# Optimization experiments

Measured on AMD Instinct MI355X. Metric: run time of the kernel, lower is better.

The kernel has to match this reference:

```python
import jax, jax.numpy as jnp
import numpy as np

GRID = (160, 160, 160)
RADIUS_FACTOR = 3.0
PATCH = 20      # fixed patch edge; covers ceil(c+r)-floor(c-r)+1 for r <= 9 voxels
CHUNK = 500
N_POINTS = 25000


def _quat_to_rot(q):
    # normalized quaternion -> rotation matrix (matches torch reference)
    q = q / jnp.clip(jnp.linalg.norm(q, axis=-1, keepdims=True), 1e-6)
    w, x, y, z = q[..., 0], q[..., 1], q[..., 2], q[..., 3]
    ww, xx, yy, zz = w * w, x * x, y * y, z * z
    wx, wy, wz = w * x, w * y, w * z
    xy, xz, yz = x * y, x * z, y * z
    r0 = jnp.stack([ww + xx - yy - zz, 2 * (xy - wz), 2 * (xz + wy)], -1)
    r1 = jnp.stack([2 * (xy + wz), ww - xx + yy - zz, 2 * (yz - wx)], -1)
    r2 = jnp.stack([2 * (xz - wy), 2 * (yz + wx), ww - xx - yy + zz], -1)
    return jnp.stack([r0, r1, r2], -2)


def setup_inputs():
    key = jax.random.key(0)
    k1, k2, k3, k4 = jax.random.split(key, 4)
    centers = jax.random.uniform(k1, (N_POINTS, 3), dtype=jnp.float32)
    # scales in [1.5, 3.0] voxels -> patch radius = 3*max(scale) <= 9 < PATCH/2
    log_scales = jnp.log(jax.random.uniform(k2, (N_POINTS, 3), minval=1.5, maxval=3.0, dtype=jnp.float32))
    quats = jax.random.normal(k3, (N_POINTS, 4), dtype=jnp.float32)
    rho = 0.1 * jax.random.normal(k4, (N_POINTS, 2), dtype=jnp.float32)  # (real, imag)
    return {"centers": centers, "log_scales": log_scales, "quats": quats, "rho": rho}


def _splat(centers, log_scales, quats, rho):
    D, H, W = GRID
    span = jnp.array([D - 1, H - 1, W - 1], jnp.float32)
    scales = jnp.exp(log_scales)                                  # [N,3]
    R = _quat_to_rot(quats)                                       # [N,3,3]
    inv = 1.0 / jnp.clip(scales, 1e-4) ** 2                       # diag of S^-2
    prec = jnp.einsum('nij,nj,nkj->nik', R, inv, R)               # R diag R^T, [N,3,3]
    cv = centers * span                                           # voxel-space centers
    rad = jnp.max(scales, axis=-1) * RADIUS_FACTOR                # per-point patch radius
    base = jnp.floor(cv - rad[:, None]).astype(jnp.int32)         # zmin/ymin/xmin (pre-clip)
    hi = jnp.ceil(cv + rad[:, None]).astype(jnp.int32)            # zmax/ymax/xmax (pre-clip)
    amp_mag = jnp.sqrt(rho[:, 0] ** 2 + rho[:, 1] ** 2)
    valid = (amp_mag >= 1e-6) & (rad >= 1e-3)                     # torch skip conditions
    dims = jnp.array([D, H, W], jnp.int32)

    nchunk = N_POINTS // CHUNK
    ck = lambda a: a.reshape((nchunk, CHUNK) + a.shape[1:])
    xs = (ck(cv), ck(base), ck(hi), ck(prec), ck(rho), ck(valid))
    offs = jnp.arange(PATCH, dtype=jnp.int32)

    def step(vol, x):
        cv_c, base_c, hi_c, p, rho_c, val_c = x
        idx = base_c[:, :, None] + offs                           # [C,3,P] voxel indices
        d = idx.astype(jnp.float32) - cv_c[:, :, None]            # [C,3,P] rel coords
        m = (idx >= 0) & (idx < dims[None, :, None]) & (idx <= hi_c[:, :, None])
        dz, dy, dx = d[:, 0], d[:, 1], d[:, 2]                    # [C,P] each
        # exponent = rel^T prec rel, built separably (prec is symmetric)
        e = ((p[:, 0, 0, None] * dz * dz)[:, :, None, None]
             + (p[:, 1, 1, None] * dy * dy)[:, None, :, None]
             + (p[:, 2, 2, None] * dx * dx)[:, None, None, :]
             + (2.0 * p[:, 0, 1, None, None] * dz[:, :, None] * dy[:, None, :])[:, :, :, None]
             + (2.0 * p[:, 0, 2, None, None] * dz[:, :, None] * dx[:, None, :])[:, :, None, :]
             + (2.0 * p[:, 1, 2, None, None] * dy[:, :, None] * dx[:, None, :])[:, None, :, :])
        w = jnp.exp(-0.5 * e)                                     # [C,P,P,P]
        mask = (m[:, 0, :, None, None] & m[:, 1, None, :, None] & m[:, 2, None, None, :]
                & val_c[:, None, None, None])
        w = jnp.where(mask, w, 0.0)
        iz = jnp.clip(idx[:, 0], 0, D - 1)
        iy = jnp.clip(idx[:, 1], 0, H - 1)
        ix = jnp.clip(idx[:, 2], 0, W - 1)
        lin = (iz[:, :, None, None] * H + iy[:, None, :, None]) * W + ix[:, None, None, :]
        contrib = w[..., None] * rho_c[:, None, None, None, :]    # [C,P,P,P,2] (re,im)
        vol = vol.at[lin.reshape(-1)].add(contrib.reshape(-1, 2))
        return vol, None

    vol, _ = jax.lax.scan(step, jnp.zeros((D * H * W, 2), jnp.float32), xs)
    return vol.reshape(D, H, W, 2)


def reference(centers, log_scales, quats, rho):
    return _splat(centers, log_scales, quats, rho)
```

## Files before the change

kernel.cpp:

```cpp
#include <hip/hip_runtime.h>


namespace {
constexpr int GD = 160, GH = 160, GW = 160;
constexpr int NPTS = 25000;
constexpr int PATCH = 20;
constexpr int TS  = 8;
constexpr int TPD = GD / TS;
constexpr int NT  = TPD * TPD * TPD;
constexpr int CAP = 384;
constexpr int PSTRIDE = 16;
constexpr float L2E = 1.4426950408889634f;
}


__global__ __launch_bounds__(256) void prep_bin(
    const float* __restrict__ centers,
    const float* __restrict__ log_scales,
    const float* __restrict__ quats,
    const float* __restrict__ rho,
    float* __restrict__ params,
    int* __restrict__ counts,
    unsigned short* __restrict__ list)
{
    const int t = blockIdx.x * 256 + threadIdx.x;
    const int gid  = t >> 6;
    const int lane = t & 63;

    const float r0 = rho[gid * 2 + 0];
    const float r1 = rho[gid * 2 + 1];
    const float s0 = __expf(log_scales[gid * 3 + 0]);
    const float s1 = __expf(log_scales[gid * 3 + 1]);
    const float s2 = __expf(log_scales[gid * 3 + 2]);

    const float smax = fmaxf(s0, fmaxf(s1, s2));
    const float rad  = smax * 3.0f;
    const float amp2 = r0 * r0 + r1 * r1;

    const float cvz = centers[gid * 3 + 0] * (float)(GD - 1);
    const float cvy = centers[gid * 3 + 1] * (float)(GH - 1);
    const float cvx = centers[gid * 3 + 2] * (float)(GW - 1);

    const int bz = (int)floorf(cvz - rad);
    const int by = (int)floorf(cvy - rad);
    const int bx = (int)floorf(cvx - rad);
    const int hz = (int)ceilf(cvz + rad);
    const int hy = (int)ceilf(cvy + rad);
    const int hx = (int)ceilf(cvx + rad);

    const int loz = max(bz, 0), upz = min(min(hz, GD - 1), bz + PATCH - 1);
    const int loy = max(by, 0), upy = min(min(hy, GH - 1), by + PATCH - 1);
    const int lox = max(bx, 0), upx = min(min(hx, GW - 1), bx + PATCH - 1);

    const bool valid = (amp2 >= 1e-12f) && (rad >= 1e-3f) &&
                       (upz >= loz) && (upy >= loy) && (upx >= lox);

    const float q0 = quats[gid * 4 + 0], q1 = quats[gid * 4 + 1];
    const float q2 = quats[gid * 4 + 2], q3 = quats[gid * 4 + 3];
    float qn = sqrtf(q0 * q0 + q1 * q1 + q2 * q2 + q3 * q3);
    qn = fmaxf(qn, 1e-6f);
    const float w = q0 / qn, x = q1 / qn, y = q2 / qn, z = q3 / qn;

    const float R00 = w * w + x * x - y * y - z * z;
    const float R01 = 2.f * (x * y - w * z);
    const float R02 = 2.f * (x * z + w * y);
    const float R10 = 2.f * (x * y + w * z);
    const float R11 = w * w - x * x + y * y - z * z;
    const float R12 = 2.f * (y * z - w * x);
    const float R20 = 2.f * (x * z - w * y);
    const float R21 = 2.f * (y * z + w * x);
    const float R22 = w * w - x * x - y * y + z * z;

    const float c0 = fmaxf(s0, 1e-4f); const float i0 = 1.f / (c0 * c0);
    const float c1 = fmaxf(s1, 1e-4f); const float i1 = 1.f / (c1 * c1);
    const float c2 = fmaxf(s2, 1e-4f); const float i2 = 1.f / (c2 * c2);

    const float p00 = R00 * R00 * i0 + R01 * R01 * i1 + R02 * R02 * i2;
    const float p01 = R00 * R10 * i0 + R01 * R11 * i1 + R02 * R12 * i2;
    const float p02 = R00 * R20 * i0 + R01 * R21 * i1 + R02 * R22 * i2;
    const float p11 = R10 * R10 * i0 + R11 * R11 * i1 + R12 * R12 * i2;
    const float p12 = R10 * R20 * i0 + R11 * R21 * i1 + R12 * R22 * i2;
    const float p22 = R20 * R20 * i0 + R21 * R21 * i1 + R22 * R22 * i2;

    const float q00s = -0.5f * L2E * p00;
    const float v    = __builtin_amdgcn_exp2f(2.f * q00s);

    const int zl = valid ? loz : 255, zu = valid ? upz : 0;
    const int yl = valid ? loy : 255, yu = valid ? upy : 0;
    const int xl = valid ? lox : 255, xu = valid ? upx : 0;
    const int loPack = zl | (yl << 8) | (xl << 16) | (zu << 24);
    const int upPack = yu | (xu << 8);

    if (lane == 0) {
        float4* P = reinterpret_cast<float4*>(params + (size_t)gid * PSTRIDE);
        P[0] = make_float4(q00s, -L2E * p01, -L2E * p02, -0.5f * L2E * p11);
        P[1] = make_float4(-L2E * p12, -0.5f * L2E * p22, cvz, cvy);
        P[2] = make_float4(cvx, r0, r1, __int_as_float(loPack));
        P[3] = make_float4(__int_as_float(upPack), v, 0.f, 0.f);
    }

    if (!valid) return;

    const int tz0 = loz >> 3, tz1 = upz >> 3;
    const int ty0 = loy >> 3, ty1 = upy >> 3;
    const int tx0 = lox >> 3, tx1 = upx >> 3;
    const int tz = tz0 + (lane >> 4);
    const int ty = ty0 + ((lane >> 2) & 3);
    const int tx = tx0 + (lane & 3);
    if (tz > tz1 || ty > ty1 || tx > tx1) return;
    const int tile = (tz * TPD + ty) * TPD + tx;
    const int pos = atomicAdd(&counts[tile], 1);
    if (pos < CAP) list[(size_t)tile * CAP + pos] = (unsigned short)gid;
}

__global__ __launch_bounds__(256, 8) void gather(
    const float* __restrict__ params,
    const int* __restrict__ counts,
    const unsigned short* __restrict__ list,
    float2* __restrict__ out)
{
    const int wli  = threadIdx.x >> 6;
    const int lane = threadIdx.x & 63;
    const int tile = blockIdx.x * 4 + wli;
    const int tz = tile / (TPD * TPD);
    const int rem = tile - tz * (TPD * TPD);
    const int ty = rem / TPD;
    const int tx = rem - ty * TPD;

    const int ly = lane >> 3, lx = lane & 7;
    const int iy = ty * TS + ly;
    const int ix = tx * TS + lx;
    const int z0 = tz * TS;
    const float fy = (float)iy, fx = (float)ix, fz = (float)z0;

    __shared__ float4 sP[4][64][4];

    int cnt = __builtin_amdgcn_readfirstlane(counts[tile]);
    if (cnt > CAP) cnt = CAP;
    const float4* p4 = reinterpret_cast<const float4*>(params);
    const unsigned short* tl = list + (size_t)tile * CAP;

    float ar[8], ai[8];
#pragma unroll
    for (int i = 0; i < 8; ++i) { ar[i] = 0.f; ai[i] = 0.f; }

    for (int b0 = 0; b0 < cnt; b0 += 64) {
        const int nb = min(64, cnt - b0);
        if (lane < nb) {
            const int g = tl[b0 + lane];
            const float4* src = p4 + (size_t)g * 4;
            sP[wli][lane][0] = src[0];
            sP[wli][lane][1] = src[1];
            sP[wli][lane][2] = src[2];
            sP[wli][lane][3] = src[3];
        }
        for (int g = 0; g < nb; ++g) {
            const float4 Pa = sP[wli][g][0];
            const float4 Pb = sP[wli][g][1];
            const float4 Pc = sP[wli][g][2];
            const float2 Pd = *reinterpret_cast<const float2*>(&sP[wli][g][3]);
            const int lo = __builtin_amdgcn_readfirstlane(__float_as_int(Pc.w));
            const int up = __builtin_amdgcn_readfirstlane(__float_as_int(Pd.x));
            const int loy_ = (lo >> 8) & 255, lox_ = (lo >> 16) & 255;
            const int upy_ = up & 255,        upx_ = (up >> 8) & 255;
            const int zl = (lo & 255) - z0;
            const int zu = ((lo >> 24) & 255) - z0;
            const bool yx = (iy >= loy_) & (iy <= upy_) &
                            (ix >= lox_) & (ix <= upx_);

            const float dy = fy - Pb.w;
            const float dx = fx - Pc.x;
            const float C = fmaf(dy, fmaf(Pa.w, dy, Pb.x * dx), Pb.y * dx * dx);
            const float B = fmaf(Pa.y, dy, Pa.z * dx);
            const float dz = fz - Pb.z;
            const float t0 = fmaf(dz, fmaf(Pa.x, dz, B), C);
            const float dt = fmaf(Pa.x, fmaf(2.f, dz, 1.f), B);
            float wgt = __builtin_amdgcn_exp2f(t0);
            float u   = __builtin_amdgcn_exp2f(dt);
            const float v = Pd.y;
            const float r0m = yx ? Pc.y : 0.f;
            const float r1m = yx ? Pc.z : 0.f;
#pragma unroll
            for (int i = 0; i < 8; ++i) {
                const float wm = (i >= zl && i <= zu) ? wgt : 0.f;
                ar[i] = fmaf(wm, r0m, ar[i]);
                ai[i] = fmaf(wm, r1m, ai[i]);
                wgt *= u;
                u *= v;
            }
        }
    }

#pragma unroll
    for (int i = 0; i < 8; ++i)
        out[((size_t)(z0 + i) * GH + iy) * GW + ix] = make_float2(ar[i], ai[i]);
}

extern "C" void kernel_launch(void* const* d_in, const int* in_sizes, int n_in,
                              void* d_out, int out_size, void* d_ws, size_t ws_size,
                              hipStream_t stream) {
    const float* centers    = (const float*)d_in[0];
    const float* log_scales = (const float*)d_in[1];
    const float* quats      = (const float*)d_in[2];
    const float* rho        = (const float*)d_in[3];

    float* params = (float*)d_ws;
    int* counts = (int*)(params + (size_t)NPTS * PSTRIDE);
    unsigned short* list = (unsigned short*)(counts + NT);

    hipMemsetAsync(counts, 0, NT * sizeof(int), stream);
    prep_bin<<<(NPTS * 64) / 256, 256, 0, stream>>>(centers, log_scales, quats,
                                                    rho, params, counts, list);
    gather<<<NT / 4, 256, 0, stream>>>(params, counts, list, (float2*)d_out);
}
```

Before: 174.3 us.

## Deepen gather tiles to 16 z-slices and skip out-of-range z iterations

Tiles in z grow from 8 to 16 voxels, so each wave accumulates 16 z-slices per pixel column and each gaussian's setup cost (parameter load, exp evaluations) is spread over more outputs. The per-tile list capacity rises, and occupancy hints drop to match the larger register footprint. The inner z loop now uses wave-uniform early break and skip on the gaussian's z range instead of masking every slice. The yx mask moves onto the weight. The risks are register pressure and lower occupancy, more gaussians per tile, and possible list overflow if a tile exceeds the new capacity.

```diff
diff --git a/kernel.cpp b/kernel.cpp
--- a/kernel.cpp
+++ b/kernel.cpp
@@ -5,10 +5,12 @@
 constexpr int GD = 160, GH = 160, GW = 160;
 constexpr int NPTS = 25000;
 constexpr int PATCH = 20;
-constexpr int TS  = 8;
-constexpr int TPD = GD / TS;
-constexpr int NT  = TPD * TPD * TPD;
-constexpr int CAP = 384;
+constexpr int TSZ = 16, TSY = 8, TSX = 8;
+constexpr int TPZ = GD / TSZ;
+constexpr int TPY = GH / TSY;
+constexpr int TPX = GW / TSX;
+constexpr int NT  = TPZ * TPY * TPX;
+constexpr int CAP = 736;
 constexpr int PSTRIDE = 16;
 constexpr float L2E = 1.4426950408889634f;
 }
@@ -101,19 +103,19 @@
 
     if (!valid) return;
 
-    const int tz0 = loz >> 3, tz1 = upz >> 3;
+    const int tz0 = loz >> 4, tz1 = upz >> 4;
     const int ty0 = loy >> 3, ty1 = upy >> 3;
     const int tx0 = lox >> 3, tx1 = upx >> 3;
     const int tz = tz0 + (lane >> 4);
     const int ty = ty0 + ((lane >> 2) & 3);
     const int tx = tx0 + (lane & 3);
     if (tz > tz1 || ty > ty1 || tx > tx1) return;
-    const int tile = (tz * TPD + ty) * TPD + tx;
+    const int tile = (tz * TPY + ty) * TPX + tx;
     const int pos = atomicAdd(&counts[tile], 1);
     if (pos < CAP) list[(size_t)tile * CAP + pos] = (unsigned short)gid;
 }
 
-__global__ __launch_bounds__(256, 8) void gather(
+__global__ __launch_bounds__(256, 4) void gather(
     const float* __restrict__ params,
     const int* __restrict__ counts,
     const unsigned short* __restrict__ list,
@@ -121,16 +123,16 @@
 {
     const int wli  = threadIdx.x >> 6;
     const int lane = threadIdx.x & 63;
-    const int tile = blockIdx.x * 4 + wli;
-    const int tz = tile / (TPD * TPD);
-    const int rem = tile - tz * (TPD * TPD);
-    const int ty = rem / TPD;
-    const int tx = rem - ty * TPD;
+    const int tile = __builtin_amdgcn_readfirstlane(blockIdx.x * 4 + wli);
+    const int tz = tile / (TPY * TPX);
+    const int rem = tile - tz * (TPY * TPX);
+    const int ty = rem / TPX;
+    const int tx = rem - ty * TPX;
 
     const int ly = lane >> 3, lx = lane & 7;
-    const int iy = ty * TS + ly;
-    const int ix = tx * TS + lx;
-    const int z0 = tz * TS;
+    const int iy = ty * TSY + ly;
+    const int ix = tx * TSX + lx;
+    const int z0 = tz * TSZ;
     const float fy = (float)iy, fx = (float)ix, fz = (float)z0;
 
     __shared__ float4 sP[4][64][4];
@@ -140,9 +142,9 @@
     const float4* p4 = reinterpret_cast<const float4*>(params);
     const unsigned short* tl = list + (size_t)tile * CAP;
 
-    float ar[8], ai[8];
+    float ar[16], ai[16];
 #pragma unroll
-    for (int i = 0; i < 8; ++i) { ar[i] = 0.f; ai[i] = 0.f; }
+    for (int i = 0; i < 16; ++i) { ar[i] = 0.f; ai[i] = 0.f; }
 
     for (int b0 = 0; b0 < cnt; b0 += 64) {
         const int nb = min(64, cnt - b0);
@@ -175,16 +177,17 @@
             const float dz = fz - Pb.z;
             const float t0 = fmaf(dz, fmaf(Pa.x, dz, B), C);
             const float dt = fmaf(Pa.x, fmaf(2.f, dz, 1.f), B);
-            float wgt = __builtin_amdgcn_exp2f(t0);
+            float wgt = yx ? __builtin_amdgcn_exp2f(t0) : 0.f;
             float u   = __builtin_amdgcn_exp2f(dt);
-            const float v = Pd.y;
-            const float r0m = yx ? Pc.y : 0.f;
-            const float r1m = yx ? Pc.z : 0.f;
+            const float v  = Pd.y;
+            const float r0 = Pc.y, r1 = Pc.z;
 #pragma unroll
-            for (int i = 0; i < 8; ++i) {
-                const float wm = (i >= zl && i <= zu) ? wgt : 0.f;
-                ar[i] = fmaf(wm, r0m, ar[i]);
-                ai[i] = fmaf(wm, r1m, ai[i]);
+            for (int i = 0; i < 16; ++i) {
+                if (i > zu) break;
+                if (i >= zl) {
+                    ar[i] = fmaf(wgt, r0, ar[i]);
+                    ai[i] = fmaf(wgt, r1, ai[i]);
+                }
                 wgt *= u;
                 u *= v;
             }
@@ -192,7 +195,7 @@
     }
 
 #pragma unroll
-    for (int i = 0; i < 8; ++i)
+    for (int i = 0; i < 16; ++i)
         out[((size_t)(z0 + i) * GH + iy) * GW + ix] = make_float2(ar[i], ai[i]);
 }
 
```

Measured after the change: 265.7 us. 1.52x slower.

## Vectorize z-recurrence with packed f32 ops and fast path for full-range points

Applied to the files above, without the earlier changes.

The gather inner loop now processes two z-slices per step with v_pk_fma_f32/v_pk_mul_f32. A stride-2 geometric recurrence uses precomputed v^2 and v^4, stored in a widened 20-float parameter record with duplicated rho values. A branch skips per-slice z masking when a gaussian covers the whole tile depth. Launch bounds drop from 8 to 6 waves per SIMD to give the packed code more registers, which may reduce occupancy, and the larger record increases LDS and global traffic.

```diff
diff --git a/kernel.cpp b/kernel.cpp
--- a/kernel.cpp
+++ b/kernel.cpp
@@ -9,8 +9,21 @@
 constexpr int TPD = GD / TS;
 constexpr int NT  = TPD * TPD * TPD;
 constexpr int CAP = 384;
-constexpr int PSTRIDE = 16;
+constexpr int PSTRIDE = 20;
 constexpr float L2E = 1.4426950408889634f;
+}
+
+typedef float f32x2 __attribute__((ext_vector_type(2)));
+
+__device__ __forceinline__ f32x2 pk_mul(f32x2 a, f32x2 b) {
+    f32x2 d;
+    asm("v_pk_mul_f32 %0, %1, %2" : "=v"(d) : "v"(a), "v"(b));
+    return d;
+}
+__device__ __forceinline__ f32x2 pk_fma(f32x2 a, f32x2 b, f32x2 c) {
+    f32x2 d;
+    asm("v_pk_fma_f32 %0, %1, %2, %3" : "=v"(d) : "v"(a), "v"(b), "v"(c));
+    return d;
 }
 
 
@@ -84,6 +97,8 @@
 
     const float q00s = -0.5f * L2E * p00;
     const float v    = __builtin_amdgcn_exp2f(2.f * q00s);
+    const float v2   = v * v;
+    const float v4   = v2 * v2;
 
     const int zl = valid ? loz : 255, zu = valid ? upz : 0;
     const int yl = valid ? loy : 255, yu = valid ? upy : 0;
@@ -95,8 +110,9 @@
         float4* P = reinterpret_cast<float4*>(params + (size_t)gid * PSTRIDE);
         P[0] = make_float4(q00s, -L2E * p01, -L2E * p02, -0.5f * L2E * p11);
         P[1] = make_float4(-L2E * p12, -0.5f * L2E * p22, cvz, cvy);
-        P[2] = make_float4(cvx, r0, r1, __int_as_float(loPack));
-        P[3] = make_float4(__int_as_float(upPack), v, 0.f, 0.f);
+        P[2] = make_float4(cvx, __int_as_float(loPack), __int_as_float(upPack), v);
+        P[3] = make_float4(r0, r0, r1, r1);
+        P[4] = make_float4(v2, 0.f, v4, v4);
     }
 
     if (!valid) return;
@@ -113,7 +129,7 @@
     if (pos < CAP) list[(size_t)tile * CAP + pos] = (unsigned short)gid;
 }
 
-__global__ __launch_bounds__(256, 8) void gather(
+__global__ __launch_bounds__(256, 6) void gather(
     const float* __restrict__ params,
     const int* __restrict__ counts,
     const unsigned short* __restrict__ list,
@@ -133,34 +149,39 @@
     const int z0 = tz * TS;
     const float fy = (float)iy, fx = (float)ix, fz = (float)z0;
 
-    __shared__ float4 sP[4][64][4];
+    __shared__ float4 sP[4][64][5];
 
     int cnt = __builtin_amdgcn_readfirstlane(counts[tile]);
     if (cnt > CAP) cnt = CAP;
     const float4* p4 = reinterpret_cast<const float4*>(params);
     const unsigned short* tl = list + (size_t)tile * CAP;
 
-    float ar[8], ai[8];
-#pragma unroll
-    for (int i = 0; i < 8; ++i) { ar[i] = 0.f; ai[i] = 0.f; }
+    f32x2 Ar[4], Ai[4];
+#pragma unroll
+    for (int i = 0; i < 4; ++i) {
+        Ar[i].x = 0.f; Ar[i].y = 0.f;
+        Ai[i].x = 0.f; Ai[i].y = 0.f;
+    }
 
     for (int b0 = 0; b0 < cnt; b0 += 64) {
         const int nb = min(64, cnt - b0);
         if (lane < nb) {
             const int g = tl[b0 + lane];
-            const float4* src = p4 + (size_t)g * 4;
+            const float4* src = p4 + (size_t)g * 5;
             sP[wli][lane][0] = src[0];
             sP[wli][lane][1] = src[1];
             sP[wli][lane][2] = src[2];
             sP[wli][lane][3] = src[3];
+            sP[wli][lane][4] = src[4];
         }
         for (int g = 0; g < nb; ++g) {
             const float4 Pa = sP[wli][g][0];
             const float4 Pb = sP[wli][g][1];
             const float4 Pc = sP[wli][g][2];
-            const float2 Pd = *reinterpret_cast<const float2*>(&sP[wli][g][3]);
-            const int lo = __builtin_amdgcn_readfirstlane(__float_as_int(Pc.w));
-            const int up = __builtin_amdgcn_readfirstlane(__float_as_int(Pd.x));
+            const float4 Pd = sP[wli][g][3];
+            const float4 Pe = sP[wli][g][4];
+            const int lo = __builtin_amdgcn_readfirstlane(__float_as_int(Pc.y));
+            const int up = __builtin_amdgcn_readfirstlane(__float_as_int(Pc.z));
             const int loy_ = (lo >> 8) & 255, lox_ = (lo >> 16) & 255;
             const int upy_ = up & 255,        upx_ = (up >> 8) & 255;
             const int zl = (lo & 255) - z0;
@@ -175,25 +196,46 @@
             const float dz = fz - Pb.z;
             const float t0 = fmaf(dz, fmaf(Pa.x, dz, B), C);
             const float dt = fmaf(Pa.x, fmaf(2.f, dz, 1.f), B);
-            float wgt = __builtin_amdgcn_exp2f(t0);
-            float u   = __builtin_amdgcn_exp2f(dt);
-            const float v = Pd.y;
-            const float r0m = yx ? Pc.y : 0.f;
-            const float r1m = yx ? Pc.z : 0.f;
-#pragma unroll
-            for (int i = 0; i < 8; ++i) {
-                const float wm = (i >= zl && i <= zu) ? wgt : 0.f;
-                ar[i] = fmaf(wm, r0m, ar[i]);
-                ai[i] = fmaf(wm, r1m, ai[i]);
-                wgt *= u;
-                u *= v;
+            const float w0 = __builtin_amdgcn_exp2f(t0);
+            const float u0 = __builtin_amdgcn_exp2f(dt);
+            const float w0m = yx ? w0 : 0.f;
+
+            const float s0 = u0 * u0 * Pc.w;
+            const float s1 = s0 * Pe.x;
+            f32x2 W;  W.x = w0m; W.y = w0m * u0;
+            f32x2 S;  S.x = s0;  S.y = s1;
+            f32x2 R0; R0.x = Pd.x; R0.y = Pd.y;
+            f32x2 R1; R1.x = Pd.z; R1.y = Pd.w;
+            f32x2 V4; V4.x = Pe.z; V4.y = Pe.w;
+
+            if (zl <= 0 && zu >= 7) {
+#pragma unroll
+                for (int k = 0; k < 4; ++k) {
+                    Ar[k] = pk_fma(W, R0, Ar[k]);
+                    Ai[k] = pk_fma(W, R1, Ai[k]);
+                    if (k < 3) { W = pk_mul(W, S); S = pk_mul(S, V4); }
+                }
+            } else {
+#pragma unroll
+                for (int k = 0; k < 4; ++k) {
+                    f32x2 WM;
+                    WM.x = (2 * k     >= zl && 2 * k     <= zu) ? W.x : 0.f;
+                    WM.y = (2 * k + 1 >= zl && 2 * k + 1 <= zu) ? W.y : 0.f;
+                    Ar[k] = pk_fma(WM, R0, Ar[k]);
+                    Ai[k] = pk_fma(WM, R1, Ai[k]);
+                    if (k < 3) { W = pk_mul(W, S); S = pk_mul(S, V4); }
+                }
             }
         }
     }
 
 #pragma unroll
-    for (int i = 0; i < 8; ++i)
-        out[((size_t)(z0 + i) * GH + iy) * GW + ix] = make_float2(ar[i], ai[i]);
+    for (int k = 0; k < 4; ++k) {
+        out[((size_t)(z0 + 2 * k)     * GH + iy) * GW + ix] =
+            make_float2(Ar[k].x, Ai[k].x);
+        out[((size_t)(z0 + 2 * k + 1) * GH + iy) * GW + ix] =
+            make_float2(Ar[k].y, Ai[k].y);
+    }
 }
 
 extern "C" void kernel_launch(void* const* d_in, const int* in_sizes, int n_in,
```

New measurement: 167.7 us. -3.8%, faster.
